# Optimization experiments

Hardware: AMD Instinct MI355X
Metric: run time of the kernel (lower is better)

## Reference

```python
import jax, jax.numpy as jnp
import numpy as np

D_MODEL = 1024
D_HIDDEN = 512
L, B = 2048, 16


def setup_inputs() -> dict:
    key = jax.random.key(0)
    ks = jax.random.split(key, 6)
    s = 0.02
    return {
        "x": jax.random.normal(ks[0], (L, B, D_MODEL), jnp.float32),
        "W1": jax.random.normal(ks[1], (D_MODEL, D_HIDDEN), jnp.float32) * s,
        "W2": jax.random.normal(ks[2], (D_HIDDEN, 2 * D_HIDDEN), jnp.float32) * s,
        "W3": jax.random.normal(ks[3], (D_HIDDEN, 3 * D_MODEL), jnp.float32) * s,
        "v": jax.random.normal(ks[4], (2, D_MODEL), jnp.float32) * s,  # v_f, v_r
        "b": jnp.zeros((2, D_MODEL), jnp.float32),                     # b_f, b_r
    }


def reference(x, W1, W2, W3, v, b):
    # ---- SRU++ attention projection ----
    # query / residual projection: [L,B,p]
    q = jnp.einsum("lbd,dp->lbp", x, W1)
    kv = jnp.einsum("lbp,pq->lbq", q, W2)
    k, va = jnp.split(kv, 2, axis=-1)                      # each [L,B,p]
    scale = 1.0 / jnp.sqrt(jnp.asarray(D_HIDDEN, x.dtype))
    scores = jnp.einsum("lbp,mbp->blm", q, k) * scale      # [B,L,L]
    attn = jax.nn.softmax(scores, axis=-1)
    ctx = jnp.einsum("blm,mbp->lbp", attn, va)             # [L,B,p]
    U = jnp.einsum("lbp,pk->lbk", ctx + q, W3)             # [L,B,3*d]
    x_tilde, f_raw, r_raw = jnp.split(U, 3, axis=-1)       # each [L,B,d]

    # ---- elementwise highway recurrence over time ----
    vf, vr = v[0], v[1]
    bf, br = b[0], b[1]

    def step(c, inp):
        xt, fr, rr, xres = inp
        f = jax.nn.sigmoid(fr + vf * c + bf)
        r = jax.nn.sigmoid(rr + vr * c + br)
        c_new = f * c + (1.0 - f) * xt
        h = r * c_new + (1.0 - r) * xres
        return c_new, h

    c0 = jnp.zeros((B, D_MODEL), x.dtype)
    _, h = jax.lax.scan(step, c0, (x_tilde, f_raw, r_raw, x))
    return h  # [L,B,d_model]
```

## Files before the change

kernel.cpp:

```cpp
#include <hip/hip_runtime.h>

typedef unsigned short u16;
typedef unsigned int u32;
typedef __attribute__((ext_vector_type(8))) short short8;
typedef __attribute__((ext_vector_type(4))) float f32x4;

__device__ __forceinline__ float b2f(u16 h) {
  union { u32 u; float f; } v; v.u = ((u32)h) << 16; return v.f;
}
__device__ __forceinline__ u16 f2b(float f) {
  union { float f; u32 u; } v; v.f = f;
  u32 u = v.u;
  u += 0x7fffu + ((u >> 16) & 1u);
  return (u16)(u >> 16);
}
__device__ __forceinline__ short8 ld8f(const float* p) {
  short8 r;
  #pragma unroll
  for (int i = 0; i < 8; i++) r[i] = (short)f2b(p[i]);
  return r;
}

__device__ __forceinline__ void gload16(const u16* g, u16* lds_wave_base) {
  __builtin_amdgcn_global_load_lds(
      (const __attribute__((address_space(1))) u32*)g,
      (__attribute__((address_space(3))) u32*)lds_wave_base, 16, 0, 0);
}

template<int EPI, int AF32>
__global__ __launch_bounds__(256)
void gemm_nt(const void* __restrict__ Av, int lda, int a_boff,
             const u16* __restrict__ Bt, int ldb, int b_boff,
             u16* __restrict__ C, int ldc, int c_boff,
             int K,
             float* __restrict__ rowsum, int rs_boff,
             const u16* __restrict__ Q, int ldq, int q_boff,
             float expscale)
{
  __shared__ __align__(16) u16 As[128 * 32];
  __shared__ __align__(16) u16 Bs[128 * 32];
  const int z = blockIdx.z;
  Bt += (size_t)z * b_boff;
  C  += (size_t)z * c_boff;
  const int row0 = blockIdx.x * 128;
  const int col0 = blockIdx.y * 128;
  const int t = threadIdx.x;
  const int lane = t & 63, wave = t >> 6;
  const int wm = (wave >> 1) * 64, wn = (wave & 1) * 64;
  const int quad = lane >> 4, lrow = lane & 15;

  f32x4 acc[4][4] = {};

  const size_t a_base = (size_t)z * a_boff + (size_t)(row0 + (t >> 2)) * lda + (t & 3) * 8;
  const float* Agf = (const float*)Av + a_base;
  const u16*   Agh = (const u16*)Av + a_base;
  const u16* Bg = Bt + (size_t)(col0 + (t >> 2)) * ldb + (t & 3) * 8;
  const size_t a64 = (size_t)64 * lda, b64 = (size_t)64 * ldb;
  u16* AsW = As + wave * 512;
  u16* BsW = Bs + wave * 512;
  u16* AsP = As + t * 8;
  u16* BsP = Bs + t * 8;

  for (int k0 = 0; k0 < K; k0 += 32) {
    if (AF32) {
      short8 ta0 = ld8f(Agf);
      short8 ta1 = ld8f(Agf + a64);
      Agf += 32;
      short8 tb0 = *(const short8*)Bg;
      short8 tb1 = *(const short8*)(Bg + b64);
      Bg += 32;
      __syncthreads();
      *(short8*)AsP = ta0;
      *(short8*)(AsP + 2048) = ta1;
      *(short8*)BsP = tb0;
      *(short8*)(BsP + 2048) = tb1;
      __syncthreads();
    } else {
      __syncthreads();
      gload16(Agh,       AsW);
      gload16(Agh + a64, AsW + 2048);
      gload16(Bg,        BsW);
      gload16(Bg + b64,  BsW + 2048);
      Agh += 32; Bg += 32;
      __syncthreads();
    }
    short8 af[4], bfr[4];
    #pragma unroll
    for (int i = 0; i < 4; i++)
      af[i] = *(const short8*)(As + (wm + i * 16 + lrow) * 32 + quad * 8);
    #pragma unroll
    for (int j = 0; j < 4; j++)
      bfr[j] = *(const short8*)(Bs + (wn + j * 16 + lrow) * 32 + quad * 8);
    #pragma unroll
    for (int i = 0; i < 4; i++)
      #pragma unroll
      for (int j = 0; j < 4; j++)
        acc[i][j] = __builtin_amdgcn_mfma_f32_16x16x32_bf16(af[i], bfr[j], acc[i][j], 0, 0, 0);
  }

  if (EPI == 0) {
    #pragma unroll
    for (int i = 0; i < 4; i++)
      #pragma unroll
      for (int r = 0; r < 4; r++) {
        size_t grow = (size_t)(row0 + wm + i * 16 + quad * 4 + r) * ldc;
        #pragma unroll
        for (int j = 0; j < 4; j++)
          C[grow + col0 + wn + j * 16 + lrow] = f2b(acc[i][j][r]);
      }
  } else if (EPI == 1) {
    #pragma unroll
    for (int i = 0; i < 4; i++)
      #pragma unroll
      for (int r = 0; r < 4; r++) {
        int lr = row0 + wm + i * 16 + quad * 4 + r;
        size_t grow = (size_t)lr * ldc;
        float s = 0.f;
        #pragma unroll
        for (int j = 0; j < 4; j++) {
          float aa = acc[i][j][r] * expscale;
          aa = fminf(fmaxf(aa, -30.f), 30.f);
          float e = exp2f(aa);
          C[grow + col0 + wn + j * 16 + lrow] = f2b(e);
          s += e;
        }
        s += __shfl_xor(s, 1, 64);
        s += __shfl_xor(s, 2, 64);
        s += __shfl_xor(s, 4, 64);
        s += __shfl_xor(s, 8, 64);
        if (lrow == 0) atomicAdd(&rowsum[(size_t)z * rs_boff + lr], s);
      }
  } else if (EPI == 2) {
    const float* rs = rowsum + (size_t)z * rs_boff;
    const u16* Qb = Q + (size_t)z * q_boff;
    #pragma unroll
    for (int i = 0; i < 4; i++)
      #pragma unroll
      for (int r = 0; r < 4; r++) {
        int lr = row0 + wm + i * 16 + quad * 4 + r;
        float inv = 1.0f / rs[lr];
        size_t growc = (size_t)lr * ldc;
        size_t growq = (size_t)lr * ldq;
        #pragma unroll
        for (int j = 0; j < 4; j++) {
          int gcol = col0 + wn + j * 16 + lrow;
          float v = acc[i][j][r] * inv + b2f(Qb[growq + gcol]);
          C[growc + gcol] = f2b(v);
        }
      }
  } else {
    #pragma unroll
    for (int i = 0; i < 4; i++)
      #pragma unroll
      for (int r = 0; r < 4; r++) {
        size_t grow = (size_t)(row0 + wm + i * 16 + quad * 4 + r) * ldc;
        #pragma unroll
        for (int j = 0; j < 4; j++) {
          int gcol = col0 + wn + j * 16 + lrow;
          int ocol = gcol < 1024 ? gcol
                                 : 1024 + 2 * (gcol & 1023) + ((gcol >> 10) - 1);
          C[grow + ocol] = f2b(acc[i][j][r]);
        }
      }
  }
}

__global__ __launch_bounds__(256)
void transpose_f32_bf16(const float* __restrict__ in, int instride,
                        u16* __restrict__ out, int outstride)
{
  __shared__ u16 tile[64][66];
  const int r0 = blockIdx.x * 64, c0 = blockIdx.y * 64;
  const int tx = threadIdx.x & 63, ty = threadIdx.x >> 6;
  #pragma unroll
  for (int i = 0; i < 64; i += 4)
    tile[ty + i][tx] = f2b(in[(size_t)(r0 + ty + i) * instride + c0 + tx]);
  __syncthreads();
  #pragma unroll
  for (int i = 0; i < 64; i += 4)
    out[(size_t)(c0 + ty + i) * outstride + r0 + tx] = tile[tx][ty + i];
}

__global__ __launch_bounds__(64)
void scan_kernel(const u16* __restrict__ U, const float* __restrict__ X,
                 const float* __restrict__ V, const float* __restrict__ Bv,
                 float* __restrict__ out)
{
  const int idx = blockIdx.x * 64 + threadIdx.x;
  const int d = idx & 1023, b = idx >> 10;
  const float nl2e = -1.4426950408889634f;
  const float vf = V[d],  vr = V[1024 + d];
  const float bf_ = Bv[d], br_ = Bv[1024 + d];
  const float pvf = nl2e * vf, pvr = nl2e * vr;

  constexpr int PF = 16;
  const size_t ustep = 16 * 3072;
  const size_t gstep = 16 * 1536;
  const size_t xstep = 16 * 1024;

  const u16*  Uxt = U + (size_t)b * 3072 + d;
  const u32*  Ug  = (const u32*)(U + (size_t)b * 3072 + 1024) + d;
  const float* Xp = X + (size_t)b * 1024 + d;
  float*       Op = out + (size_t)b * 1024 + d;

  u16 pxt[PF]; u32 pg[PF]; float pxr[PF];
  #pragma unroll
  for (int p = 0; p < PF; p++) {
    pxt[p] = Uxt[0];
    pg[p]  = Ug[0];
    pxr[p] = Xp[0];
    Uxt += ustep; Ug += gstep; Xp += xstep;
  }

  float c = 0.f;
  for (int l0 = 0; l0 < 2048 - PF; l0 += PF) {
    #pragma unroll
    for (int p = 0; p < PF; p++) {
      float xt = b2f(pxt[p]);
      u32 g = pg[p];
      float fr = b2f((u16)(g & 0xffffu));
      float rr = b2f((u16)(g >> 16));
      float xr = pxr[p];
      pxt[p] = Uxt[0];
      pg[p]  = Ug[0];
      pxr[p] = Xp[0];
      Uxt += ustep; Ug += gstep; Xp += xstep;
      float ef = __builtin_amdgcn_exp2f(fmaf(pvf, c, nl2e * (fr + bf_)));
      float er = __builtin_amdgcn_exp2f(fmaf(pvr, c, nl2e * (rr + br_)));
      float fg = __builtin_amdgcn_rcpf(1.f + ef);
      float rg = __builtin_amdgcn_rcpf(1.f + er);
      c = fg * (c - xt) + xt;
      float h = rg * (c - xr) + xr;
      Op[0] = h; Op += xstep;
      __builtin_amdgcn_sched_barrier(0);
    }
  }
  #pragma unroll
  for (int p = 0; p < PF; p++) {
    float xt = b2f(pxt[p]);
    u32 g = pg[p];
    float fr = b2f((u16)(g & 0xffffu));
    float rr = b2f((u16)(g >> 16));
    float xr = pxr[p];
    float ef = __builtin_amdgcn_exp2f(fmaf(pvf, c, nl2e * (fr + bf_)));
    float er = __builtin_amdgcn_exp2f(fmaf(pvr, c, nl2e * (rr + br_)));
    float fg = __builtin_amdgcn_rcpf(1.f + ef);
    float rg = __builtin_amdgcn_rcpf(1.f + er);
    c = fg * (c - xt) + xt;
    float h = rg * (c - xr) + xr;
    Op[0] = h; Op += xstep;
  }
}

extern "C" void kernel_launch(void* const* d_in, const int* in_sizes, int n_in,
                              void* d_out, int out_size, void* d_ws, size_t ws_size,
                              hipStream_t stream) {
  const float* x  = (const float*)d_in[0];
  const float* W1 = (const float*)d_in[1];
  const float* W2 = (const float*)d_in[2];
  const float* W3 = (const float*)d_in[3];
  const float* v  = (const float*)d_in[4];
  const float* bb = (const float*)d_in[5];
  float* out = (float*)d_out;
  char* ws = (char*)d_ws;

  u16*   E      = (u16*)(ws + 0);
  u16*   q      = (u16*)(ws + 134217728);
  u16*   vat    = (u16*)(ws + 167772160);
  u16*   kbuf   = (u16*)(ws + 201326592);
  u16*   ctxq   = (u16*)(ws + 201326592);
  float* rowsum = (float*)(ws + 234881024);
  u16*   W1t    = (u16*)(ws + 235012096);
  u16*   W2t    = (u16*)(ws + 236060672);
  u16*   W3t    = (u16*)(ws + 237109248);
  u16*   U      = (u16*)(ws + 0);

  hipMemsetAsync(rowsum, 0, 131072, stream);

  const dim3 blk(256);
  transpose_f32_bf16<<<dim3(16, 8),  blk, 0, stream>>>(W1, 512,  W1t, 1024);
  transpose_f32_bf16<<<dim3(8, 16),  blk, 0, stream>>>(W2, 1024, W2t, 512);
  transpose_f32_bf16<<<dim3(8, 48),  blk, 0, stream>>>(W3, 3072, W3t, 512);

  gemm_nt<0, 1><<<dim3(256, 4, 1), blk, 0, stream>>>(x, 1024, 0, W1t, 1024, 0,
                                                     q, 512, 0, 1024,
                                                     nullptr, 0, nullptr, 0, 0, 0.f);
  gemm_nt<0, 0><<<dim3(256, 4, 1), blk, 0, stream>>>(q, 512, 0, W2t, 512, 0,
                                                     kbuf, 512, 0, 512,
                                                     nullptr, 0, nullptr, 0, 0, 0.f);
  gemm_nt<0, 0><<<dim3(4, 16, 16), blk, 0, stream>>>(W2t + 262144, 512, 0, q, 8192, 512,
                                                     vat, 2048, 1048576, 512,
                                                     nullptr, 0, nullptr, 0, 0, 0.f);
  const float expscale = 0.044194173824159216f * 1.4426950408889634f;
  gemm_nt<1, 0><<<dim3(16, 16, 16), blk, 0, stream>>>(q, 8192, 512, kbuf, 8192, 512,
                                                      E, 2048, 4194304, 512,
                                                      rowsum, 2048, nullptr, 0, 0, expscale);
  gemm_nt<2, 0><<<dim3(16, 4, 16), blk, 0, stream>>>(E, 2048, 4194304, vat, 2048, 1048576,
                                                     ctxq, 8192, 512, 2048,
                                                     rowsum, 2048, q, 8192, 512, 0.f);
  gemm_nt<3, 0><<<dim3(256, 24, 1), blk, 0, stream>>>(ctxq, 512, 0, W3t, 512, 0,
                                                      U, 3072, 0, 512,
                                                      nullptr, 0, nullptr, 0, 0, 0.f);
  scan_kernel<<<dim3(256, 1, 1), dim3(64), 0, stream>>>(U, x, v, bb, out);
}
```

Baseline: 1.030 ms.

## Double-buffer LDS tiles with async global_load_lds prefetch in bf16 GEMM path

Splits the GEMM main loop by input type. The bf16 path now uses two LDS buffers, issuing direct global-to-LDS loads two k-tiles ahead and waiting with explicit vmcnt counts, so global memory latency overlaps with MFMA work. This doubles LDS use per block, which may lower occupancy, and it relies on hand-placed waitcnt and barrier ordering being correct. The fp32-input path keeps its original single-buffer behaviour.

New measurement: 999.0 us. 3.0% less time.

```diff
diff --git a/kernel.cpp b/kernel.cpp
--- a/kernel.cpp
+++ b/kernel.cpp
@@ -37,8 +37,8 @@
              const u16* __restrict__ Q, int ldq, int q_boff,
              float expscale)
 {
-  __shared__ __align__(16) u16 As[128 * 32];
-  __shared__ __align__(16) u16 Bs[128 * 32];
+  __shared__ __align__(16) u16 As[2 * 4096];
+  __shared__ __align__(16) u16 Bs[2 * 4096];
   const int z = blockIdx.z;
   Bt += (size_t)z * b_boff;
   C  += (size_t)z * c_boff;
@@ -56,46 +56,82 @@
   const u16*   Agh = (const u16*)Av + a_base;
   const u16* Bg = Bt + (size_t)(col0 + (t >> 2)) * ldb + (t & 3) * 8;
   const size_t a64 = (size_t)64 * lda, b64 = (size_t)64 * ldb;
-  u16* AsW = As + wave * 512;
-  u16* BsW = Bs + wave * 512;
-  u16* AsP = As + t * 8;
-  u16* BsP = Bs + t * 8;
-
-  for (int k0 = 0; k0 < K; k0 += 32) {
-    if (AF32) {
-      short8 ta0 = ld8f(Agf);
-      short8 ta1 = ld8f(Agf + a64);
-      Agf += 32;
-      short8 tb0 = *(const short8*)Bg;
-      short8 tb1 = *(const short8*)(Bg + b64);
-      Bg += 32;
+
+  if constexpr (!AF32) {
+    const int nt = K >> 5;
+    u16* AsW = As + wave * 512;
+    u16* BsW = Bs + wave * 512;
+    auto stage = [&](int buf, int s) {
+      const u16* a = Agh + (size_t)s * 32;
+      const u16* b = Bg  + (size_t)s * 32;
+      u16* aw = AsW + buf * 4096;
+      u16* bw = BsW + buf * 4096;
+      gload16(a,       aw);
+      gload16(a + a64, aw + 2048);
+      gload16(b,       bw);
+      gload16(b + b64, bw + 2048);
+    };
+    stage(0, 0);
+    stage(1, 1);
+    for (int kt = 0; kt < nt; ++kt) {
+      const int cur = kt & 1;
+      if (kt < nt - 1) {
+        asm volatile("s_waitcnt vmcnt(4)" ::: "memory");
+      } else {
+        asm volatile("s_waitcnt vmcnt(0)" ::: "memory");
+      }
+      __builtin_amdgcn_sched_barrier(0);
+      __builtin_amdgcn_s_barrier();
+      const u16* Ab = As + cur * 4096;
+      const u16* Bb = Bs + cur * 4096;
+      short8 af[4], bfr[4];
+      #pragma unroll
+      for (int i = 0; i < 4; i++)
+        af[i] = *(const short8*)(Ab + (wm + i * 16 + lrow) * 32 + quad * 8);
+      #pragma unroll
+      for (int j = 0; j < 4; j++)
+        bfr[j] = *(const short8*)(Bb + (wn + j * 16 + lrow) * 32 + quad * 8);
+      #pragma unroll
+      for (int i = 0; i < 4; i++)
+        #pragma unroll
+        for (int j = 0; j < 4; j++)
+          acc[i][j] = __builtin_amdgcn_mfma_f32_16x16x32_bf16(af[i], bfr[j], acc[i][j], 0, 0, 0);
+      asm volatile("" ::: "memory");
+      __builtin_amdgcn_sched_barrier(0);
+      __builtin_amdgcn_s_barrier();
+      if (kt + 2 < nt) stage(cur, kt + 2);
+    }
+  } else {
+    u16* AsP = As + t * 8;
+    u16* BsP = Bs + t * 8;
+    const u16* BgP = Bg;
+    const float* AgfP = Agf;
+    for (int k0 = 0; k0 < K; k0 += 32) {
+      short8 ta0 = ld8f(AgfP);
+      short8 ta1 = ld8f(AgfP + a64);
+      AgfP += 32;
+      short8 tb0 = *(const short8*)BgP;
+      short8 tb1 = *(const short8*)(BgP + b64);
+      BgP += 32;
       __syncthreads();
       *(short8*)AsP = ta0;
       *(short8*)(AsP + 2048) = ta1;
       *(short8*)BsP = tb0;
       *(short8*)(BsP + 2048) = tb1;
       __syncthreads();
-    } else {
-      __syncthreads();
-      gload16(Agh,       AsW);
-      gload16(Agh + a64, AsW + 2048);
-      gload16(Bg,        BsW);
-      gload16(Bg + b64,  BsW + 2048);
-      Agh += 32; Bg += 32;
-      __syncthreads();
+      short8 af[4], bfr[4];
+      #pragma unroll
+      for (int i = 0; i < 4; i++)
+        af[i] = *(const short8*)(As + (wm + i * 16 + lrow) * 32 + quad * 8);
+      #pragma unroll
+      for (int j = 0; j < 4; j++)
+        bfr[j] = *(const short8*)(Bs + (wn + j * 16 + lrow) * 32 + quad * 8);
+      #pragma unroll
+      for (int i = 0; i < 4; i++)
+        #pragma unroll
+        for (int j = 0; j < 4; j++)
+          acc[i][j] = __builtin_amdgcn_mfma_f32_16x16x32_bf16(af[i], bfr[j], acc[i][j], 0, 0, 0);
     }
-    short8 af[4], bfr[4];
-    #pragma unroll
-    for (int i = 0; i < 4; i++)
-      af[i] = *(const short8*)(As + (wm + i * 16 + lrow) * 32 + quad * 8);
-    #pragma unroll
-    for (int j = 0; j < 4; j++)
-      bfr[j] = *(const short8*)(Bs + (wn + j * 16 + lrow) * 32 + quad * 8);
-    #pragma unroll
-    for (int i = 0; i < 4; i++)
-      #pragma unroll
-      for (int j = 0; j < 4; j++)
-        acc[i][j] = __builtin_amdgcn_mfma_f32_16x16x32_bf16(af[i], bfr[j], acc[i][j], 0, 0, 0);
   }
 
   if (EPI == 0) {
```
